# Optimization experiments

Measured on AMD Instinct MI355X. Metric: run time of the kernel, lower is better.

The kernel has to match this reference:

```python
import jax, jax.numpy as jnp
import numpy as np
from jax import lax

N, H, W = 16, 112, 112
CIN, COUT, K = 256, 256, 3
STRIDE, PAD = 1, 1


def setup_inputs() -> dict:
    key = jax.random.key(0)
    kx, kw = jax.random.split(key)
    # int8-valued activations and weights, stored as int32 for portable integer conv
    x = jax.random.randint(kx, (N, H, W, CIN), -128, 128, dtype=jnp.int32)
    # weight layout matches the torch module: (out_channels, kH, kW, in_channels) == OHWI
    weight = jax.random.randint(kw, (COUT, K, K, CIN), -128, 128, dtype=jnp.int32)
    return {"x": x, "weight": weight}


def reference(x, weight):
    y = lax.conv_general_dilated(
        x,
        weight,
        window_strides=(STRIDE, STRIDE),
        padding=[(PAD, PAD), (PAD, PAD)],
        dimension_numbers=("NHWC", "OHWI", "NHWC"),
        preferred_element_type=jnp.int32,
    )
    return y  # (N, H, W, COUT) int32
```

## Files before the change

kernel.cpp:

```cpp
#include <hip/hip_runtime.h>
#include <stdint.h>

#define NN   16
#define HH   112
#define WW   112
#define CIN  256
#define COUT 256
#define HP   114
#define WP   114
#define M_TOTAL (NN * HH * WW)
#define XP_BYTES ((size_t)NN * HP * WP * CIN)
#define WPK_BYTES ((size_t)9 * COUT * CIN)

typedef int v4i __attribute__((ext_vector_type(4)));

__device__ __forceinline__ void load_lds16(const void* g, void* l) {
  __builtin_amdgcn_global_load_lds(
      (const __attribute__((address_space(1))) void*)g,
      (__attribute__((address_space(3))) void*)l, 16, 0, 0);
}

__device__ __forceinline__ int pack4(int a, int b, int c, int d) {
  return (a & 255) | ((b & 255) << 8) | ((c & 255) << 16) | (d << 24);
}

__global__ void pack_x_kernel(const int* __restrict__ x, char* __restrict__ xp) {
  int t = blockIdx.x * 256 + threadIdx.x;
  int g = t & 15;
  int p = t >> 4;
  int w = p % WW;
  int t2 = p / WW;
  int h = t2 % HH;
  int n = t2 / HH;
  const int4* src = (const int4*)(x + (size_t)t * 16);
  int4 a = src[0], b = src[1], c = src[2], d = src[3];
  int4 ov;
  ov.x = pack4(a.x, a.y, a.z, a.w);
  ov.y = pack4(b.x, b.y, b.z, b.w);
  ov.z = pack4(c.x, c.y, c.z, c.w);
  ov.w = pack4(d.x, d.y, d.z, d.w);
  size_t dst = (((size_t)n * HP + (h + 1)) * WP + (w + 1)) * CIN + (size_t)g * 16;
  *(int4*)(xp + dst) = ov;
}

__global__ void pack_w_border_kernel(const int* __restrict__ wgt, char* __restrict__ xp,
                                     char* __restrict__ wp) {
  int bid = blockIdx.x;
  if (bid < 576) {
    int t = bid * 256 + threadIdx.x;
    int c4 = t & 63;
    int r = t >> 6;
    int tap = r % 9;
    int cout = r / 9;
    int4 v = *(const int4*)(wgt + (size_t)t * 4);
    int ov = pack4(v.x, v.y, v.z, v.w);
    size_t dst = ((size_t)tap * COUT + cout) * CIN + (size_t)c4 * 4;
    *(int*)(wp + dst) = ov;
  } else {
    int t = (bid - 576) * 256 + threadIdx.x;
    int g = t & 15;
    int pix = t >> 4;
    int n = pix / 452;
    int b = pix % 452;
    int h, w;
    if (b < 114) { h = 0; w = b; }
    else if (b < 228) { h = 113; w = b - 114; }
    else { int r = b - 228; h = 1 + (r >> 1); w = (r & 1) ? 113 : 0; }
    size_t dst = (((size_t)n * HP + h) * WP + w) * CIN + (size_t)g * 16;
    *(int4*)(xp + dst) = make_int4(0, 0, 0, 0);
  }
}

__global__ __launch_bounds__(256, 2) void conv_mfma_kernel(const char* __restrict__ xp,
                                                           const char* __restrict__ wp,
                                                           int* __restrict__ out) {
  __shared__ __align__(16) char As[3 * 128 * 64];
  __shared__ __align__(16) char Bs[3 * 256 * 64];
  const int tid = threadIdx.x;
  const int lane = tid & 63;
  const int wave = tid >> 6;
  const int mtile = blockIdx.x;

  const char* gptr[6];
  char* lptr[6];
  int  isA[6];
#pragma unroll
  for (int j = 0; j < 6; j++) {
    int c = wave * 6 + j;
    if (c < 8) {
      int row = c * 16 + (lane >> 2);
      int colg = (lane & 3) ^ ((row >> 1) & 3);
      int m = mtile * 128 + row;
      int w = m % WW;
      int t2 = m / WW;
      int h = t2 % HH;
      int n = t2 / HH;
      gptr[j] = xp + (((size_t)n * HP + h) * WP + w) * CIN + (size_t)colg * 16;
      lptr[j] = As + c * 1024;
      isA[j] = 1;
    } else {
      int cb = c - 8;
      int row = cb * 16 + (lane >> 2);
      int colg = (lane & 3) ^ ((row >> 1) & 3);
      gptr[j] = wp + (size_t)row * CIN + (size_t)colg * 16;
      lptr[j] = Bs + cb * 1024;
      isA[j] = 0;
    }
  }

  const int wm = wave & 1;
  const int wn = wave >> 1;
  int aoff[4], boff[8];
#pragma unroll
  for (int i = 0; i < 4; i++) {
    int ra = wm * 64 + i * 16 + (lane & 15);
    aoff[i] = ra * 64 + (((lane >> 4) ^ ((ra >> 1) & 3)) * 16);
  }
#pragma unroll
  for (int j = 0; j < 8; j++) {
    int rb = wn * 128 + j * 16 + (lane & 15);
    boff[j] = rb * 64 + (((lane >> 4) ^ ((rb >> 1) & 3)) * 16);
  }

  v4i acc[4][8];
#pragma unroll
  for (int i = 0; i < 4; i++)
#pragma unroll
    for (int j = 0; j < 8; j++) acc[i][j] = (v4i){0, 0, 0, 0};

  auto stage_half = [&](int ks, int b, int half) {
    int tap = ks >> 2;
    int kb = ks & 3;
    int ky = tap / 3;
    int kx = tap - ky * 3;
    int offA = (ky * WP + kx) * CIN + kb * 64;
    int offB = tap * (COUT * CIN) + kb * 64;
#pragma unroll
    for (int j = half * 3; j < half * 3 + 3; j++)
      load_lds16(gptr[j] + (isA[j] ? offA : offB),
                 lptr[j] + (isA[j] ? b * 8192 : b * 16384));
  };

  stage_half(0, 0, 0); stage_half(0, 0, 1);
  stage_half(1, 1, 0); stage_half(1, 1, 1);
  asm volatile("s_waitcnt vmcnt(6)" ::: "memory");
  __builtin_amdgcn_s_barrier();

  int bc = 0;
  int bs = 2;
#pragma unroll 1
  for (int ks = 0; ks < 36; ks++) {
    const char* Ab = As + bc * 8192;
    const char* Bb = Bs + bc * 16384;
    v4i af[4], bf[8];

#pragma unroll
    for (int i = 0; i < 4; i++) af[i] = *(const v4i*)(Ab + aoff[i]);
#pragma unroll
    for (int j = 0; j < 4; j++) bf[j] = *(const v4i*)(Bb + boff[j]);
    if (ks < 34) stage_half(ks + 2, bs, 0);
    __builtin_amdgcn_s_barrier();
    asm volatile("s_waitcnt lgkmcnt(0)" ::: "memory");
    __builtin_amdgcn_s_setprio(1);
#pragma unroll
    for (int i = 0; i < 4; i++)
#pragma unroll
      for (int j = 0; j < 4; j++)
        acc[i][j] = __builtin_amdgcn_mfma_i32_16x16x64_i8(af[i], bf[j], acc[i][j], 0, 0, 0);
    __builtin_amdgcn_s_setprio(0);
    __builtin_amdgcn_s_barrier();

#pragma unroll
    for (int j = 4; j < 8; j++) bf[j] = *(const v4i*)(Bb + boff[j]);
    if (ks < 34) stage_half(ks + 2, bs, 1);
    __builtin_amdgcn_s_barrier();
    asm volatile("s_waitcnt lgkmcnt(0)" ::: "memory");
    __builtin_amdgcn_s_setprio(1);
#pragma unroll
    for (int i = 0; i < 4; i++)
#pragma unroll
      for (int j = 4; j < 8; j++)
        acc[i][j] = __builtin_amdgcn_mfma_i32_16x16x64_i8(af[i], bf[j], acc[i][j], 0, 0, 0);
    __builtin_amdgcn_s_setprio(0);

    if (ks < 34)       asm volatile("s_waitcnt vmcnt(6)" ::: "memory");
    else if (ks == 34) asm volatile("s_waitcnt vmcnt(0)" ::: "memory");
    __builtin_amdgcn_s_barrier();

    bc = (bc == 2) ? 0 : bc + 1;
    bs = (bs == 2) ? 0 : bs + 1;
  }

#pragma unroll
  for (int i = 0; i < 4; i++) {
    const int mg = mtile * 128 + wm * 64 + i * 16 + ((lane >> 4) * 4);
#pragma unroll
    for (int r = 0; r < 4; r++) {
      int* orow = out + (size_t)(mg + r) * COUT + wn * 128 + (lane & 15);
#pragma unroll
      for (int j = 0; j < 8; j++) orow[j * 16] = acc[i][j][r];
    }
  }
}

__global__ void conv_naive_kernel(const int* __restrict__ x, const int* __restrict__ wgt,
                                  int* __restrict__ out, int total) {
  int idx = blockIdx.x * 256 + threadIdx.x;
  if (idx >= total) return;
  int co = idx & 255;
  int p = idx >> 8;
  int w = p % WW;
  int t2 = p / WW;
  int h = t2 % HH;
  int n = t2 / HH;
  int acc = 0;
  for (int ky = 0; ky < 3; ky++) {
    int ih = h + ky - 1;
    if (ih < 0 || ih >= HH) continue;
    for (int kx = 0; kx < 3; kx++) {
      int iw = w + kx - 1;
      if (iw < 0 || iw >= WW) continue;
      const int* xs = x + (((size_t)n * HH + ih) * WW + iw) * CIN;
      const int* ws = wgt + ((size_t)co * 9 + ky * 3 + kx) * CIN;
      for (int ci = 0; ci < CIN; ci++) acc += xs[ci] * ws[ci];
    }
  }
  out[idx] = acc;
}

extern "C" void kernel_launch(void* const* d_in, const int* in_sizes, int n_in,
                              void* d_out, int out_size, void* d_ws, size_t ws_size,
                              hipStream_t stream) {
  const int* x = (const int*)d_in[0];
  const int* wgt = (const int*)d_in[1];
  int* out = (int*)d_out;
  const size_t need = XP_BYTES + WPK_BYTES;
  if (ws_size >= need) {
    char* xp = (char*)d_ws;
    char* wp = xp + XP_BYTES;
    pack_x_kernel<<<(M_TOTAL * 16) / 256, 256, 0, stream>>>(x, xp);
    pack_w_border_kernel<<<576 + 452, 256, 0, stream>>>(wgt, xp, wp);
    conv_mfma_kernel<<<M_TOTAL / 128, 256, 0, stream>>>(xp, wp, out);
  } else {
    conv_naive_kernel<<<(out_size + 255) / 256, 256, 0, stream>>>(x, wgt, out, out_size);
  }
}
```

Before: 465.5 us.

## Load A operand directly from global into registers, drop A LDS staging

Activation (A) tiles are no longer staged through LDS. Each lane gathers its MFMA A fragments straight from global memory into a double-buffered register array, one k-step ahead. Only weights (B) still go through the LDS triple buffer. The k-loop is unrolled by 6 with a single barrier per step instead of three, and all 32 MFMAs of a step are issued together. This saves LDS space and LDS traffic and cuts synchronisation, at the cost of more VGPRs and global-load latency exposed on the register path.

```diff
diff --git a/kernel.cpp b/kernel.cpp
--- a/kernel.cpp
+++ b/kernel.cpp
@@ -18,6 +18,12 @@
   __builtin_amdgcn_global_load_lds(
       (const __attribute__((address_space(1))) void*)g,
       (__attribute__((address_space(3))) void*)l, 16, 0, 0);
+}
+
+__device__ __forceinline__ void bar() {
+  asm volatile("" ::: "memory");
+  __builtin_amdgcn_s_barrier();
+  asm volatile("" ::: "memory");
 }
 
 __device__ __forceinline__ int pack4(int a, int b, int c, int d) {
@@ -74,48 +80,37 @@
 __global__ __launch_bounds__(256, 2) void conv_mfma_kernel(const char* __restrict__ xp,
                                                            const char* __restrict__ wp,
                                                            int* __restrict__ out) {
-  __shared__ __align__(16) char As[3 * 128 * 64];
   __shared__ __align__(16) char Bs[3 * 256 * 64];
   const int tid = threadIdx.x;
   const int lane = tid & 63;
   const int wave = tid >> 6;
   const int mtile = blockIdx.x;
-
-  const char* gptr[6];
-  char* lptr[6];
-  int  isA[6];
-#pragma unroll
-  for (int j = 0; j < 6; j++) {
-    int c = wave * 6 + j;
-    if (c < 8) {
-      int row = c * 16 + (lane >> 2);
-      int colg = (lane & 3) ^ ((row >> 1) & 3);
-      int m = mtile * 128 + row;
-      int w = m % WW;
-      int t2 = m / WW;
-      int h = t2 % HH;
-      int n = t2 / HH;
-      gptr[j] = xp + (((size_t)n * HP + h) * WP + w) * CIN + (size_t)colg * 16;
-      lptr[j] = As + c * 1024;
-      isA[j] = 1;
-    } else {
-      int cb = c - 8;
-      int row = cb * 16 + (lane >> 2);
-      int colg = (lane & 3) ^ ((row >> 1) & 3);
-      gptr[j] = wp + (size_t)row * CIN + (size_t)colg * 16;
-      lptr[j] = Bs + cb * 1024;
-      isA[j] = 0;
-    }
-  }
-
   const int wm = wave & 1;
   const int wn = wave >> 1;
-  int aoff[4], boff[8];
+
+  const char* gptrB[4];
+  char* lptrB[4];
+#pragma unroll
+  for (int j = 0; j < 4; j++) {
+    int c = wave * 4 + j;
+    int row = c * 16 + (lane >> 2);
+    int colg = (lane & 3) ^ ((row >> 1) & 3);
+    gptrB[j] = wp + (size_t)row * CIN + (size_t)colg * 16;
+    lptrB[j] = Bs + c * 1024;
+  }
+
+  const char* abase[4];
 #pragma unroll
   for (int i = 0; i < 4; i++) {
-    int ra = wm * 64 + i * 16 + (lane & 15);
-    aoff[i] = ra * 64 + (((lane >> 4) ^ ((ra >> 1) & 3)) * 16);
-  }
+    int ra = mtile * 128 + wm * 64 + i * 16 + (lane & 15);
+    int w = ra % WW;
+    int t2 = ra / WW;
+    int h = t2 % HH;
+    int n = t2 / HH;
+    abase[i] = xp + (((size_t)n * HP + h) * WP + w) * CIN + (size_t)(lane >> 4) * 16;
+  }
+
+  int boff[8];
 #pragma unroll
   for (int j = 0; j < 8; j++) {
     int rb = wn * 128 + j * 16 + (lane & 15);
@@ -128,68 +123,64 @@
 #pragma unroll
     for (int j = 0; j < 8; j++) acc[i][j] = (v4i){0, 0, 0, 0};
 
-  auto stage_half = [&](int ks, int b, int half) {
+  auto stageB = [&](int ks, int b) {
+    int tap = ks >> 2;
+    int kb = ks & 3;
+    int offB = tap * (COUT * CIN) + kb * 64;
+#pragma unroll
+    for (int j = 0; j < 4; j++) load_lds16(gptrB[j] + offB, lptrB[j] + b * 16384);
+  };
+  auto gatherA = [&](int ks, v4i* dst) {
     int tap = ks >> 2;
     int kb = ks & 3;
     int ky = tap / 3;
     int kx = tap - ky * 3;
-    int offA = (ky * WP + kx) * CIN + kb * 64;
-    int offB = tap * (COUT * CIN) + kb * 64;
-#pragma unroll
-    for (int j = half * 3; j < half * 3 + 3; j++)
-      load_lds16(gptr[j] + (isA[j] ? offA : offB),
-                 lptr[j] + (isA[j] ? b * 8192 : b * 16384));
+    int off = (ky * WP + kx) * CIN + kb * 64;
+#pragma unroll
+    for (int i = 0; i < 4; i++) dst[i] = *(const v4i*)(abase[i] + off);
   };
 
-  stage_half(0, 0, 0); stage_half(0, 0, 1);
-  stage_half(1, 1, 0); stage_half(1, 1, 1);
-  asm volatile("s_waitcnt vmcnt(6)" ::: "memory");
-  __builtin_amdgcn_s_barrier();
-
-  int bc = 0;
-  int bs = 2;
+  v4i afr[2][4];
+
+  stageB(0, 0);
+  stageB(1, 1);
+  gatherA(0, afr[0]);
+  asm volatile("s_waitcnt vmcnt(8)" ::: "memory");
+  bar();
+
+#define CONV_STEP(KS, BC, CUR, NXT, DOSTAGE, DOGATHER, VMN)                         \
+  {                                                                                 \
+    const char* Bb = Bs + (BC) * 16384;                                             \
+    v4i bf[8];                                                                      \
+    _Pragma("unroll") for (int j = 0; j < 8; j++)                                   \
+        bf[j] = *(const v4i*)(Bb + boff[j]);                                        \
+    if (DOSTAGE) stageB((KS) + 2, ((BC) + 2) % 3);                                  \
+    if (DOGATHER) gatherA((KS) + 1, afr[NXT]);                                      \
+    asm volatile("s_waitcnt vmcnt(" VMN ")" ::: "memory");                          \
+    __builtin_amdgcn_s_setprio(1);                                                  \
+    _Pragma("unroll") for (int i = 0; i < 4; i++)                                   \
+      _Pragma("unroll") for (int j = 0; j < 8; j++)                                 \
+        acc[i][j] = __builtin_amdgcn_mfma_i32_16x16x64_i8(afr[CUR][i], bf[j],       \
+                                                          acc[i][j], 0, 0, 0);      \
+    __builtin_amdgcn_s_setprio(0);                                                  \
+    bar();                                                                          \
+  }
+
 #pragma unroll 1
-  for (int ks = 0; ks < 36; ks++) {
-    const char* Ab = As + bc * 8192;
-    const char* Bb = Bs + bc * 16384;
-    v4i af[4], bf[8];
-
-#pragma unroll
-    for (int i = 0; i < 4; i++) af[i] = *(const v4i*)(Ab + aoff[i]);
-#pragma unroll
-    for (int j = 0; j < 4; j++) bf[j] = *(const v4i*)(Bb + boff[j]);
-    if (ks < 34) stage_half(ks + 2, bs, 0);
-    __builtin_amdgcn_s_barrier();
-    asm volatile("s_waitcnt lgkmcnt(0)" ::: "memory");
-    __builtin_amdgcn_s_setprio(1);
-#pragma unroll
-    for (int i = 0; i < 4; i++)
-#pragma unroll
-      for (int j = 0; j < 4; j++)
-        acc[i][j] = __builtin_amdgcn_mfma_i32_16x16x64_i8(af[i], bf[j], acc[i][j], 0, 0, 0);
-    __builtin_amdgcn_s_setprio(0);
-    __builtin_amdgcn_s_barrier();
-
-#pragma unroll
-    for (int j = 4; j < 8; j++) bf[j] = *(const v4i*)(Bb + boff[j]);
-    if (ks < 34) stage_half(ks + 2, bs, 1);
-    __builtin_amdgcn_s_barrier();
-    asm volatile("s_waitcnt lgkmcnt(0)" ::: "memory");
-    __builtin_amdgcn_s_setprio(1);
-#pragma unroll
-    for (int i = 0; i < 4; i++)
-#pragma unroll
-      for (int j = 4; j < 8; j++)
-        acc[i][j] = __builtin_amdgcn_mfma_i32_16x16x64_i8(af[i], bf[j], acc[i][j], 0, 0, 0);
-    __builtin_amdgcn_s_setprio(0);
-
-    if (ks < 34)       asm volatile("s_waitcnt vmcnt(6)" ::: "memory");
-    else if (ks == 34) asm volatile("s_waitcnt vmcnt(0)" ::: "memory");
-    __builtin_amdgcn_s_barrier();
-
-    bc = (bc == 2) ? 0 : bc + 1;
-    bs = (bs == 2) ? 0 : bs + 1;
-  }
+  for (int it = 0; it < 5; it++) {
+    int base = it * 6;
+#pragma unroll
+    for (int u = 0; u < 6; u++) {
+      CONV_STEP(base + u, u % 3, u & 1, (u + 1) & 1, true, true, "8")
+    }
+  }
+  CONV_STEP(30, 0, 0, 1, true,  true,  "8")
+  CONV_STEP(31, 1, 1, 0, true,  true,  "8")
+  CONV_STEP(32, 2, 0, 1, true,  true,  "8")
+  CONV_STEP(33, 0, 1, 0, true,  true,  "8")
+  CONV_STEP(34, 1, 0, 1, false, true,  "4")
+  CONV_STEP(35, 2, 1, 0, false, false, "0")
+#undef CONV_STEP
 
 #pragma unroll
   for (int i = 0; i < 4; i++) {
```

Measured after the change: 571.3 us. 22.7% more time.
